# Optimization experiments

Measured on AMD Instinct MI355X. Metric: run time of the kernel, lower is better.

The kernel has to match this reference:

```python
import jax, jax.numpy as jnp
import numpy as np

L, H, Wn, C = 2048, 768, 1024, 64


def setup_inputs() -> dict:
    key = jax.random.key(0)
    ks = jax.random.split(key, 12)
    s = 1.0 / np.sqrt(H)
    s3 = 1.0 / np.sqrt(3 * H)
    return {
        "tok_embs": jax.random.normal(ks[0], (L, H), jnp.float32),
        "wmask": jax.random.randint(ks[1], (L,), 0, Wn + 1),  # 1-indexed word positions, 0 = ignore
        "text_length": Wn,
        "label_embs": jax.random.normal(ks[2], (C, H), jnp.float32),
        "W_tok": jax.random.normal(ks[3], (H, 2 * H), jnp.float32) * s,
        "b_tok": jnp.zeros((2 * H,), jnp.float32),
        "W_lab": jax.random.normal(ks[4], (H, 2 * H), jnp.float32) * s,
        "b_lab": jnp.zeros((2 * H,), jnp.float32),
        "W1": jax.random.normal(ks[5], (3 * H, H), jnp.float32) * s3,
        "b1": jnp.zeros((H,), jnp.float32),
        "W2": jax.random.normal(ks[6], (H, 3), jnp.float32) * s,
        "b2": jnp.zeros((3,), jnp.float32),
    }


def reference(tok_embs, wmask, text_length, label_embs, W_tok, b_tok, W_lab, b_lab, W1, b1, W2, b2):
    Wd = text_length
    Hd = tok_embs.shape[-1]
    # --- word-level scatter pooling: we[wmask-1] = tok_embs where wmask > 0 ---
    # route masked-out tokens to a dummy row Wd, then drop it (jit-safe, no nonzero)
    tgt = jnp.where(wmask > 0, wmask - 1, Wd)
    we = jnp.zeros((Wd + 1, Hd), tok_embs.dtype).at[tgt].set(tok_embs)[:Wd]  # (W, H)
    # --- scorer ---
    t = (we @ W_tok + b_tok).reshape(Wd, 2, Hd)        # (W, 2, H)
    lb = (label_embs @ W_lab + b_lab).reshape(-1, 2, Hd)  # (C, 2, H)
    Cd = lb.shape[0]
    t0 = jnp.broadcast_to(t[:, None, 0, :], (Wd, Cd, Hd))
    l0 = jnp.broadcast_to(lb[None, :, 0, :], (Wd, Cd, Hd))
    prod = t[:, None, 1, :] * lb[None, :, 1, :]        # (W, C, H)
    cat = jnp.concatenate([t0, l0, prod], axis=-1)     # (W, C, 3H)
    h = jax.nn.relu(cat @ W1 + b1)                     # (W, C, H)
    scores = h @ W2 + b2                               # (W, C, 3)
    return scores
```

## Files before the change

kernel.cpp:

```cpp
#include <hip/hip_runtime.h>
#include <hip/hip_bf16.h>

static constexpr int Hd = 768;
static constexpr int H2 = 1536;
static constexpr int Cn = 64;

typedef __attribute__((ext_vector_type(8))) short short8;
typedef __attribute__((ext_vector_type(8))) _Float16 half8;
typedef __attribute__((ext_vector_type(4))) float f32x4;
typedef unsigned short us;

__device__ inline unsigned int f2bf2(float a, float b) {
    __hip_bfloat162 h = __float22bfloat162_rn(float2{a, b});
    return *reinterpret_cast<unsigned int*>(&h);
}

__device__ inline void split1(float x, us& h, us& l) {
    __hip_bfloat16 hb = __float2bfloat16(x);
    float hf = __bfloat162float(hb);
    __hip_bfloat16 lb_ = __float2bfloat16(x - hf);
    h = *reinterpret_cast<us*>(&hb);
    l = *reinterpret_cast<us*>(&lb_);
}

__device__ inline us f2b(float x) {
    __hip_bfloat16 b = __float2bfloat16(x);
    return *reinterpret_cast<us*>(&b);
}

__device__ inline us f2h(float x) {
    _Float16 h = (_Float16)x;
    return *reinterpret_cast<us*>(&h);
}

__device__ inline float b2f(us u) {
    __hip_bfloat16 b = *reinterpret_cast<__hip_bfloat16*>(&u);
    return __bfloat162float(b);
}

__device__ inline short8 hmul8(short8 a, short8 b) {
    half8 x = __builtin_bit_cast(half8, a);
    half8 y = __builtin_bit_cast(half8, b);
    half8 r = x * y;
    return __builtin_bit_cast(short8, r);
}

__device__ inline void gload16(const void* g, void* l) {
    __builtin_amdgcn_global_load_lds(
        (const __attribute__((address_space(1))) unsigned int*)g,
        (__attribute__((address_space(3))) unsigned int*)l, 16, 0, 0);
}

__global__ void k_init(int* widx, int Wd) {
    int i = blockIdx.x * 256 + threadIdx.x;
    if (i < Wd) widx[i] = -1;
}

__global__ void k_scatter(const int* __restrict__ wmask, int* widx, int L, int Wd) {
    int i = blockIdx.x * 256 + threadIdx.x;
    if (i < L) {
        int m = wmask[i];
        if (m > 0 && m <= Wd) atomicMax(&widx[m - 1], i);
    }
}

__global__ void k_build_we_split(const float4* __restrict__ tok, const int* __restrict__ widx,
                                 us* __restrict__ weh, us* __restrict__ wel, int Wd) {
    int i = blockIdx.x * 256 + threadIdx.x;
    if (i >= Wd * 192) return;
    int w = i / 192, c4 = i - w * 192;
    int idx = widx[w];
    float4 v = (idx >= 0) ? tok[idx * 192 + c4] : float4{0.f, 0.f, 0.f, 0.f};
    us hh[4], ll[4];
    split1(v.x, hh[0], ll[0]);
    split1(v.y, hh[1], ll[1]);
    split1(v.z, hh[2], ll[2]);
    split1(v.w, hh[3], ll[3]);
    size_t o = (size_t)w * Hd + c4 * 4;
    *(ushort4*)&weh[o] = ushort4{hh[0], hh[1], hh[2], hh[3]};
    *(ushort4*)&wel[o] = ushort4{ll[0], ll[1], ll[2], ll[3]};
}

struct TSArgs {
    const float* src[5];
    us* th[5];
    us* tl[5];
    int ld[5];
    int N[5];
    int fmt[5];
};
__global__ __launch_bounds__(256)
void k_tsplit(TSArgs a) {
    __shared__ float tile[64][65];
    const int z = blockIdx.z;
    const int n0 = blockIdx.x * 64, k0 = blockIdx.y * 64;
    if (n0 >= a.N[z]) return;
    const float* W = a.src[z];
    const int ld = a.ld[z];
    for (int idx = threadIdx.x; idx < 4096; idx += 256) {
        int kk = idx >> 6, nn = idx & 63;
        tile[kk][nn] = W[(size_t)(k0 + kk) * ld + n0 + nn];
    }
    __syncthreads();
    us* Th = a.th[z];
    us* Tl = a.tl[z];
    const int fmt = a.fmt[z];
    for (int idx = threadIdx.x; idx < 4096; idx += 256) {
        int nn = idx >> 6, kk = idx & 63;
        size_t o = (size_t)(n0 + nn) * Hd + k0 + kk;
        if (fmt) {
            Th[o] = f2h(tile[kk][nn]);
        } else {
            us h, l;
            split1(tile[kk][nn], h, l);
            Th[o] = h;
            Tl[o] = l;
        }
    }
}

__global__ __launch_bounds__(256)
void k_split(const float* __restrict__ x, int lda, int cols,
             us* __restrict__ h, us* __restrict__ l, int n4) {
    int i = blockIdx.x * 256 + threadIdx.x;
    if (i >= n4) return;
    int c4 = cols >> 2;
    int row = i / c4, cc = (i - row * c4) * 4;
    float4 v = *(const float4*)&x[(size_t)row * lda + cc];
    us hh[4], ll[4];
    split1(v.x, hh[0], ll[0]);
    split1(v.y, hh[1], ll[1]);
    split1(v.z, hh[2], ll[2]);
    split1(v.w, hh[3], ll[3]);
    size_t o = (size_t)row * cols + cc;
    *(ushort4*)&h[o] = ushort4{hh[0], hh[1], hh[2], hh[3]};
    *(ushort4*)&l[o] = ushort4{ll[0], ll[1], ll[2], ll[3]};
}

__global__ __launch_bounds__(256)
void k_gemm2(const us* __restrict__ Ah, const us* __restrict__ Al,
             const us* __restrict__ BhT, const us* __restrict__ BlT,
             float* __restrict__ Cpart, int M, int N, int K) {
    __shared__ __align__(16) us S[2][4][64 * 32];
    const int tid = threadIdx.x, wave = tid >> 6, lane = tid & 63;
    const int quad = lane >> 4, l15 = lane & 15;
    const int wm = wave & 1, wn = wave >> 1;
    const int m0 = blockIdx.y * 64, n0 = blockIdx.x * 64;
    const int Ks = K / gridDim.z, kbeg = blockIdx.z * Ks, kend = kbeg + Ks;
    float* C = Cpart + (size_t)blockIdx.z * M * N;

    const int srow = wave * 16 + (lane >> 2), soff = (lane & 3) * 8;
    const size_t gaB = (size_t)(m0 + srow) * K + soff;
    const size_t gbB = (size_t)(n0 + srow) * K + soff;
    const int lo = wave * 16 * 32;

    f32x4 acc[2][2];
#pragma unroll
    for (int a = 0; a < 2; ++a)
#pragma unroll
        for (int b = 0; b < 2; ++b) acc[a][b] = (f32x4){0.f, 0.f, 0.f, 0.f};

    auto stage = [&](int p, int k0) {
        gload16(Ah + gaB + k0, &S[p][0][lo]);
        gload16(Al + gaB + k0, &S[p][1][lo]);
        gload16(BhT + gbB + k0, &S[p][2][lo]);
        gload16(BlT + gbB + k0, &S[p][3][lo]);
    };

    int p = 0;
    stage(0, kbeg);
    for (int k0 = kbeg; k0 < kend; k0 += 32) {
        __syncthreads();
        if (k0 + 32 < kend) stage(p ^ 1, k0 + 32);
        short8 ah[2], al[2], bh[2], bl[2];
#pragma unroll
        for (int mt = 0; mt < 2; ++mt) {
            int off = (wm * 32 + mt * 16 + l15) * 32 + quad * 8;
            ah[mt] = *(const short8*)&S[p][0][off];
            al[mt] = *(const short8*)&S[p][1][off];
        }
#pragma unroll
        for (int nt = 0; nt < 2; ++nt) {
            int off = (wn * 32 + nt * 16 + l15) * 32 + quad * 8;
            bh[nt] = *(const short8*)&S[p][2][off];
            bl[nt] = *(const short8*)&S[p][3][off];
        }
#pragma unroll
        for (int mt = 0; mt < 2; ++mt)
#pragma unroll
            for (int nt = 0; nt < 2; ++nt) {
                acc[mt][nt] = __builtin_amdgcn_mfma_f32_16x16x32_bf16(al[mt], bh[nt], acc[mt][nt], 0, 0, 0);
                acc[mt][nt] = __builtin_amdgcn_mfma_f32_16x16x32_bf16(ah[mt], bl[nt], acc[mt][nt], 0, 0, 0);
                acc[mt][nt] = __builtin_amdgcn_mfma_f32_16x16x32_bf16(ah[mt], bh[nt], acc[mt][nt], 0, 0, 0);
            }
        p ^= 1;
    }
#pragma unroll
    for (int mt = 0; mt < 2; ++mt)
#pragma unroll
        for (int nt = 0; nt < 2; ++nt) {
            int col = n0 + wn * 32 + nt * 16 + l15;
#pragma unroll
            for (int reg = 0; reg < 4; ++reg) {
                int row = m0 + wm * 32 + mt * 16 + quad * 4 + reg;
                C[(size_t)row * N + col] = acc[mt][nt][reg];
            }
        }
}

__global__ __launch_bounds__(256)
void k_gemm3(const us* __restrict__ Ah, const us* __restrict__ Al,
             const us* __restrict__ BhT, const us* __restrict__ BlT,
             const float* __restrict__ bias, float* __restrict__ outF,
             us* __restrict__ sh, us* __restrict__ sl, us* __restrict__ bh16,
             int fp16out, int scols, int N, int K) {
    __shared__ __align__(16) us S[2][4][64 * 32];
    const int tid = threadIdx.x, wave = tid >> 6, lane = tid & 63;
    const int quad = lane >> 4, l15 = lane & 15;
    const int wm = wave & 1, wn = wave >> 1;
    const int m0 = blockIdx.y * 64, n0 = blockIdx.x * 64;

    const int srow = wave * 16 + (lane >> 2), soff = (lane & 3) * 8;
    const size_t gaB = (size_t)(m0 + srow) * K + soff;
    const size_t gbB = (size_t)(n0 + srow) * K + soff;
    const int lo = wave * 16 * 32;

    f32x4 acc[2][2];
#pragma unroll
    for (int a = 0; a < 2; ++a)
#pragma unroll
        for (int b = 0; b < 2; ++b) acc[a][b] = (f32x4){0.f, 0.f, 0.f, 0.f};

    auto stage = [&](int p, int k0) {
        gload16(Ah + gaB + k0, &S[p][0][lo]);
        gload16(Al + gaB + k0, &S[p][1][lo]);
        gload16(BhT + gbB + k0, &S[p][2][lo]);
        gload16(BlT + gbB + k0, &S[p][3][lo]);
    };

    int p = 0;
    stage(0, 0);
    for (int k0 = 0; k0 < K; k0 += 32) {
        __syncthreads();
        if (k0 + 32 < K) stage(p ^ 1, k0 + 32);
        short8 ah[2], al[2], bh[2], bl[2];
#pragma unroll
        for (int mt = 0; mt < 2; ++mt) {
            int off = (wm * 32 + mt * 16 + l15) * 32 + quad * 8;
            ah[mt] = *(const short8*)&S[p][0][off];
            al[mt] = *(const short8*)&S[p][1][off];
        }
#pragma unroll
        for (int nt = 0; nt < 2; ++nt) {
            int off = (wn * 32 + nt * 16 + l15) * 32 + quad * 8;
            bh[nt] = *(const short8*)&S[p][2][off];
            bl[nt] = *(const short8*)&S[p][3][off];
        }
#pragma unroll
        for (int mt = 0; mt < 2; ++mt)
#pragma unroll
            for (int nt = 0; nt < 2; ++nt) {
                acc[mt][nt] = __builtin_amdgcn_mfma_f32_16x16x32_bf16(al[mt], bh[nt], acc[mt][nt], 0, 0, 0);
                acc[mt][nt] = __builtin_amdgcn_mfma_f32_16x16x32_bf16(ah[mt], bl[nt], acc[mt][nt], 0, 0, 0);
                acc[mt][nt] = __builtin_amdgcn_mfma_f32_16x16x32_bf16(ah[mt], bh[nt], acc[mt][nt], 0, 0, 0);
            }
        p ^= 1;
    }
#pragma unroll
    for (int mt = 0; mt < 2; ++mt)
#pragma unroll
        for (int nt = 0; nt < 2; ++nt) {
            int col = n0 + wn * 32 + nt * 16 + l15;
            float bb = bias ? bias[col] : 0.f;
#pragma unroll
            for (int reg = 0; reg < 4; ++reg) {
                int row = m0 + wm * 32 + mt * 16 + quad * 4 + reg;
                float v = acc[mt][nt][reg] + bb;
                if (outF) outF[(size_t)row * N + col] = v;
                if (sh) {
                    if (col < scols) {
                        us h, l;
                        split1(v, h, l);
                        size_t o = (size_t)row * scols + col;
                        sh[o] = h;
                        sl[o] = l;
                    } else if (bh16) {
                        bh16[(size_t)row * scols + (col - scols)] = fp16out ? f2h(v) : f2b(v);
                    }
                }
            }
        }
}

__global__ __launch_bounds__(256)
void k_reduce(const float* __restrict__ part, int S, int MN, int N,
              const float* __restrict__ bias, float* __restrict__ outF,
              us* __restrict__ sh, us* __restrict__ sl, int scols,
              us* __restrict__ bh16, int fp16out) {
    int i = blockIdx.x * 256 + threadIdx.x;
    if (i >= MN) return;
    float v = 0.f;
    for (int s = 0; s < S; ++s) v += part[(size_t)s * MN + i];
    int row = i / N, col = i - row * N;
    if (bias) v += bias[col];
    if (outF) outF[i] = v;
    if (col < scols) {
        if (sh) {
            us h, l;
            split1(v, h, l);
            size_t o = (size_t)row * scols + col;
            sh[o] = h;
            sl[o] = l;
        }
    } else if (bh16) {
        bh16[(size_t)row * scols + (col - scols)] = fp16out ? f2h(v) : f2b(v);
    }
}

__global__ __launch_bounds__(256, 2)
void k_mfma9(const us* __restrict__ t1b,
             const us* __restrict__ W1ct,
             const us* __restrict__ lb1b,
             const float* __restrict__ Aw,
             const float* __restrict__ Bc,
             const float* __restrict__ W2,
             float* __restrict__ scr) {
    __shared__ __align__(16) us As[3][4096];
    __shared__ __align__(16) us Bs[3][4096];
    __shared__ __align__(16) us lbs[2][Hd];
    __shared__ float sred[2 * 128 * 3];

    const int tid = threadIdx.x, wave = tid >> 6, lane = tid & 63;
    const int quad = lane >> 4, l15 = lane & 15;
    const int wm = wave & 1, wn = wave >> 1;

    const int b = blockIdx.x;
    const int xcd = b & 7, slot = b >> 3;
    const int jx = slot >> 5;
    const int cp = slot & 31;
    const int c0 = cp * 2;
    const int jt = jx * 128, m0 = xcd * 128;

    for (int i = tid; i < 2 * 128 * 3; i += 256) sred[i] = 0.f;
    if (tid < 192) {
        int cc = tid / 96, o = (tid - cc * 96) * 8;
        *(short8*)&lbs[cc][o] = *(const short8*)&lb1b[(size_t)(c0 + cc) * Hd + o];
    }

    const int srow = (wave & 1) * 64 + lane;
    const int skq = (wave >> 1) * 8;
    const us* gA = W1ct + (size_t)(jt + srow) * Hd + skq;
    const us* gB = t1b + (size_t)(m0 + srow) * Hd + skq;

    f32x4 acc0[4][4], acc1[4][4];
#pragma unroll
    for (int mt = 0; mt < 4; ++mt)
#pragma unroll
        for (int nt = 0; nt < 4; ++nt) {
            acc0[mt][nt] = (f32x4){0.f, 0.f, 0.f, 0.f};
            acc1[mt][nt] = (f32x4){0.f, 0.f, 0.f, 0.f};
        }

    auto stage = [&](int p, int k0) {
        gload16(gA + k0,      &As[p][wave * 512]);
        gload16(gA + k0 + 16, &As[p][(wave + 4) * 512]);
        gload16(gB + k0,      &Bs[p][wave * 512]);
        gload16(gB + k0 + 16, &Bs[p][(wave + 4) * 512]);
    };

    const int rbA = quad * 1024 + (wm * 64 + l15) * 8;
    const int rbB = quad * 1024 + (wn * 64 + l15) * 8;

    __syncthreads();

    stage(0, 0);
    stage(1, 32);
    int p = 0;
    for (int k0 = 0; k0 < Hd; k0 += 32) {
        if (k0 + 32 < Hd) asm volatile("s_waitcnt vmcnt(4)" ::: "memory");
        else              asm volatile("s_waitcnt vmcnt(0)" ::: "memory");
        __builtin_amdgcn_s_barrier();
        __builtin_amdgcn_sched_barrier(0);
        if (k0 + 64 < Hd) {
            int nb = p + 2; if (nb >= 3) nb -= 3;
            stage(nb, k0 + 64);
        }
        short8 af[4], bf[4];
#pragma unroll
        for (int mt = 0; mt < 4; ++mt) af[mt] = *(const short8*)&As[p][rbA + mt * 128];
#pragma unroll
        for (int nt = 0; nt < 4; ++nt) bf[nt] = *(const short8*)&Bs[p][rbB + nt * 128];
        short8 lv0 = *(const short8*)&lbs[0][k0 + quad * 8];
        short8 lv1 = *(const short8*)&lbs[1][k0 + quad * 8];
        __builtin_amdgcn_s_setprio(1);
#pragma unroll
        for (int mt = 0; mt < 4; ++mt) {
            short8 a0 = hmul8(af[mt], lv0);
            short8 a1 = hmul8(af[mt], lv1);
#pragma unroll
            for (int nt = 0; nt < 4; ++nt) {
                acc0[mt][nt] = __builtin_amdgcn_mfma_f32_16x16x32_f16(
                    __builtin_bit_cast(half8, a0),
                    __builtin_bit_cast(half8, bf[nt]), acc0[mt][nt], 0, 0, 0);
                acc1[mt][nt] = __builtin_amdgcn_mfma_f32_16x16x32_f16(
                    __builtin_bit_cast(half8, a1),
                    __builtin_bit_cast(half8, bf[nt]), acc1[mt][nt], 0, 0, 0);
            }
        }
        __builtin_amdgcn_s_setprio(0);
        p = (p + 1 < 3) ? p + 1 : 0;
    }

    float bcv0[4][4], bcv1[4][4], w2v[4][4][3];
#pragma unroll
    for (int mt = 0; mt < 4; ++mt) {
        const int jb = jt + wm * 64 + mt * 16 + quad * 4;
        float4 b4 = *(const float4*)&Bc[(size_t)c0 * Hd + jb];
        bcv0[mt][0] = b4.x; bcv0[mt][1] = b4.y; bcv0[mt][2] = b4.z; bcv0[mt][3] = b4.w;
        float4 b5 = *(const float4*)&Bc[(size_t)(c0 + 1) * Hd + jb];
        bcv1[mt][0] = b5.x; bcv1[mt][1] = b5.y; bcv1[mt][2] = b5.z; bcv1[mt][3] = b5.w;
#pragma unroll
        for (int reg = 0; reg < 4; ++reg)
#pragma unroll
            for (int r = 0; r < 3; ++r) w2v[mt][reg][r] = W2[(jb + reg) * 3 + r];
    }

    auto reduce_c = [&](const f32x4 (&ac)[4][4], const float (&bcv)[4][4], int cc) {
#pragma unroll
        for (int nt = 0; nt < 4; ++nt) {
            const int w = m0 + wn * 64 + nt * 16 + l15;
            const float* awp = Aw + (size_t)w * Hd + jt + wm * 64;
            float s0 = 0.f, s1 = 0.f, s2 = 0.f;
#pragma unroll
            for (int mt = 0; mt < 4; ++mt) {
                float4 a4 = *(const float4*)&awp[mt * 16 + quad * 4];
                float av[4] = {a4.x, a4.y, a4.z, a4.w};
#pragma unroll
                for (int reg = 0; reg < 4; ++reg) {
                    float h = ac[mt][nt][reg] + av[reg] + bcv[mt][reg];
                    h = h > 0.f ? h : 0.f;
                    s0 += h * w2v[mt][reg][0];
                    s1 += h * w2v[mt][reg][1];
                    s2 += h * w2v[mt][reg][2];
                }
            }
            s0 += __shfl_xor(s0, 16); s0 += __shfl_xor(s0, 32);
            s1 += __shfl_xor(s1, 16); s1 += __shfl_xor(s1, 32);
            s2 += __shfl_xor(s2, 16); s2 += __shfl_xor(s2, 32);
            if (quad == 0) {
                const int wl = wn * 64 + nt * 16 + l15;
                atomicAdd(&sred[cc * 384 + wl * 3 + 0], s0);
                atomicAdd(&sred[cc * 384 + wl * 3 + 1], s1);
                atomicAdd(&sred[cc * 384 + wl * 3 + 2], s2);
            }
        }
    };
    reduce_c(acc0, bcv0, 0);
    reduce_c(acc1, bcv1, 1);
    __syncthreads();

    float* slab = scr + ((size_t)jx * 1024 * Cn + (size_t)m0 * Cn) * 3;
    for (int i = tid; i < 2 * 128 * 3; i += 256) {
        int cc = i / 384, j = i - cc * 384;
        int wl = j / 3, r = j - wl * 3;
        slab[((size_t)wl * Cn + (c0 + cc)) * 3 + r] = sred[i];
    }
}

__global__ __launch_bounds__(256)
void k_scores(const float* __restrict__ scr, const float* __restrict__ b2,
              float* __restrict__ out, int n) {
    int i = blockIdx.x * 256 + threadIdx.x;
    if (i >= n) return;
    float v = b2[i % 3];
#pragma unroll
    for (int s = 0; s < 6; ++s) v += scr[(size_t)s * n + i];
    out[i] = v;
}

extern "C" void kernel_launch(void* const* d_in, const int* in_sizes, int n_in,
                              void* d_out, int out_size, void* d_ws, size_t ws_size,
                              hipStream_t stream) {
    const float* tok    = (const float*)d_in[0];
    const int*   wmask  = (const int*)d_in[1];
    const float* labe   = (const float*)d_in[3];
    const float* W_tok  = (const float*)d_in[4];
    const float* b_tok  = (const float*)d_in[5];
    const float* W_lab  = (const float*)d_in[6];
    const float* b_lab  = (const float*)d_in[7];
    const float* W1     = (const float*)d_in[8];
    const float* b1     = (const float*)d_in[9];
    const float* W2     = (const float*)d_in[10];
    const float* b2     = (const float*)d_in[11];
    float* out = (float*)d_out;

    const int L  = in_sizes[1];
    const int Wd = out_size / (Cn * 3);

    char* ws = (char*)d_ws;
    size_t off = 0;
    auto alloc = [&](size_t bytes) { char* p = ws + off; off += (bytes + 255) & ~(size_t)255; return p; };
    int*   widx  = (int*)alloc(4096);
    float* Abuf  = (float*)alloc((size_t)Wd * Hd * 4);
    float* Bbuf  = (float*)alloc((size_t)Cn * Hd * 4);
    us* W1ct  = (us*)alloc((size_t)Hd * Hd * 2);
    us* W1cl  = (us*)alloc((size_t)Hd * Hd * 2);
    us* t1b   = (us*)alloc((size_t)Wd * Hd * 2);
    us* lb1b  = (us*)alloc((size_t)Cn * Hd * 2);
    float* scr = (float*)alloc((size_t)6 * Wd * Cn * 3 * 4);
    us* WtTh  = (us*)alloc((size_t)H2 * Hd * 2);
    us* WtTl  = (us*)alloc((size_t)H2 * Hd * 2);
    us* WlTh  = (us*)alloc((size_t)H2 * Hd * 2);
    us* WlTl  = (us*)alloc((size_t)H2 * Hd * 2);
    us* W1aTh = (us*)alloc((size_t)Hd * Hd * 2);
    us* W1aTl = (us*)alloc((size_t)Hd * Hd * 2);
    us* W1bTh = (us*)alloc((size_t)Hd * Hd * 2);
    us* W1bTl = (us*)alloc((size_t)Hd * Hd * 2);
    us* weh   = (us*)alloc((size_t)Wd * Hd * 2);
    us* wel   = (us*)alloc((size_t)Wd * Hd * 2);
    us* lah   = (us*)alloc((size_t)Cn * Hd * 2);
    us* lal   = (us*)alloc((size_t)Cn * Hd * 2);
    us* t0h   = (us*)alloc((size_t)Wd * Hd * 2);
    us* t0l   = (us*)alloc((size_t)Wd * Hd * 2);
    us* lb0h  = (us*)alloc((size_t)Cn * Hd * 2);
    us* lb0l  = (us*)alloc((size_t)Cn * Hd * 2);
    float* part = (float*)alloc((size_t)8 * Cn * H2 * 4);

    k_init<<<(Wd + 255) / 256, 256, 0, stream>>>(widx, Wd);
    k_scatter<<<(L + 255) / 256, 256, 0, stream>>>(wmask, widx, L, Wd);
    k_build_we_split<<<(Wd * 192 + 255) / 256, 256, 0, stream>>>((const float4*)tok, widx, weh, wel, Wd);

    TSArgs ts;
    ts.src[0] = W_tok;  ts.th[0] = WtTh;  ts.tl[0] = WtTl;  ts.ld[0] = H2; ts.N[0] = H2; ts.fmt[0] = 0;
    ts.src[1] = W_lab;  ts.th[1] = WlTh;  ts.tl[1] = WlTl;  ts.ld[1] = H2; ts.N[1] = H2; ts.fmt[1] = 0;
    ts.src[2] = W1;                         ts.th[2] = W1aTh; ts.tl[2] = W1aTl; ts.ld[2] = Hd; ts.N[2] = Hd; ts.fmt[2] = 0;
    ts.src[3] = W1 + (size_t)Hd * Hd;       ts.th[3] = W1bTh; ts.tl[3] = W1bTl; ts.ld[3] = Hd; ts.N[3] = Hd; ts.fmt[3] = 0;
    ts.src[4] = W1 + (size_t)2 * Hd * Hd;   ts.th[4] = W1ct;  ts.tl[4] = W1cl;  ts.ld[4] = Hd; ts.N[4] = Hd; ts.fmt[4] = 1;
    k_tsplit<<<dim3(H2 / 64, Hd / 64, 5), 256, 0, stream>>>(ts);

    k_split<<<(Cn * Hd / 4 + 255) / 256, 256, 0, stream>>>(labe, Hd, Hd, lah, lal, Cn * Hd / 4);

    k_gemm3<<<dim3(H2 / 64, Wd / 64), 256, 0, stream>>>(weh, wel, WtTh, WtTl, b_tok,
                                                        nullptr, t0h, t0l, t1b, 1, Hd, H2, Hd);

    k_gemm2<<<dim3(H2 / 64, 1, 8), 256, 0, stream>>>(lah, lal, WlTh, WlTl, part, Cn, H2, Hd);
    k_reduce<<<(Cn * H2 + 255) / 256, 256, 0, stream>>>(part, 8, Cn * H2, H2, b_lab, nullptr, lb0h, lb0l, Hd, lb1b, 1);

    k_gemm3<<<dim3(Hd / 64, Wd / 64), 256, 0, stream>>>(t0h, t0l, W1aTh, W1aTl, nullptr,
                                                        Abuf, nullptr, nullptr, nullptr, 0, 0, Hd, Hd);

    k_gemm2<<<dim3(Hd / 64, 1, 8), 256, 0, stream>>>(lb0h, lb0l, W1bTh, W1bTl, part, Cn, Hd, Hd);
    k_reduce<<<(Cn * Hd + 255) / 256, 256, 0, stream>>>(part, 8, Cn * Hd, Hd, b1, Bbuf, nullptr, nullptr, Hd, nullptr, 0);

    k_mfma9<<<1536, 256, 0, stream>>>(t1b, W1ct, lb1b, Abuf, Bbuf, W2, scr);

    k_scores<<<(Wd * Cn * 3 + 255) / 256, 256, 0, stream>>>(scr, b2, out, Wd * Cn * 3);
}
```

Before: 259.0 us.

## Double-buffer MFMA operand fragments in registers to overlap LDS reads with compute

Restructures the fused W1c MFMA kernel's K loop into a two-stage register ping-pong. The next tile's A/B/label fragments are read from LDS, and the following global tile is staged, before the current tile's MFMA cluster runs. The goal is to hide LDS read latency behind matrix instructions. In exchange, the global wait changes from vmcnt(4) to vmcnt(0), so only one tile is prefetched ahead instead of two. The extra fragment registers also raise VGPR pressure under the two-blocks-per-CU launch bound.

```diff
diff --git a/kernel.cpp b/kernel.cpp
--- a/kernel.cpp
+++ b/kernel.cpp
@@ -318,13 +318,13 @@
 }
 
 __global__ __launch_bounds__(256, 2)
-void k_mfma9(const us* __restrict__ t1b,
-             const us* __restrict__ W1ct,
-             const us* __restrict__ lb1b,
-             const float* __restrict__ Aw,
-             const float* __restrict__ Bc,
-             const float* __restrict__ W2,
-             float* __restrict__ scr) {
+void k_mfma10(const us* __restrict__ t1b,
+              const us* __restrict__ W1ct,
+              const us* __restrict__ lb1b,
+              const float* __restrict__ Aw,
+              const float* __restrict__ Bc,
+              const float* __restrict__ W2,
+              float* __restrict__ scr) {
     __shared__ __align__(16) us As[3][4096];
     __shared__ __align__(16) us Bs[3][4096];
     __shared__ __align__(16) us lbs[2][Hd];
@@ -361,7 +361,7 @@
             acc1[mt][nt] = (f32x4){0.f, 0.f, 0.f, 0.f};
         }
 
-    auto stage = [&](int p, int k0) {
+    auto stageT = [&](int p, int k0) {
         gload16(gA + k0,      &As[p][wave * 512]);
         gload16(gA + k0 + 16, &As[p][(wave + 4) * 512]);
         gload16(gB + k0,      &Bs[p][wave * 512]);
@@ -371,32 +371,25 @@
     const int rbA = quad * 1024 + (wm * 64 + l15) * 8;
     const int rbB = quad * 1024 + (wn * 64 + l15) * 8;
 
-    __syncthreads();
-
-    stage(0, 0);
-    stage(1, 32);
-    int p = 0;
-    for (int k0 = 0; k0 < Hd; k0 += 32) {
-        if (k0 + 32 < Hd) asm volatile("s_waitcnt vmcnt(4)" ::: "memory");
-        else              asm volatile("s_waitcnt vmcnt(0)" ::: "memory");
-        __builtin_amdgcn_s_barrier();
-        __builtin_amdgcn_sched_barrier(0);
-        if (k0 + 64 < Hd) {
-            int nb = p + 2; if (nb >= 3) nb -= 3;
-            stage(nb, k0 + 64);
-        }
-        short8 af[4], bf[4];
-#pragma unroll
-        for (int mt = 0; mt < 4; ++mt) af[mt] = *(const short8*)&As[p][rbA + mt * 128];
-#pragma unroll
-        for (int nt = 0; nt < 4; ++nt) bf[nt] = *(const short8*)&Bs[p][rbB + nt * 128];
-        short8 lv0 = *(const short8*)&lbs[0][k0 + quad * 8];
-        short8 lv1 = *(const short8*)&lbs[1][k0 + quad * 8];
+    auto readFrags = [&](short8 (&af)[4], short8 (&bf)[4], short8& l0, short8& l1,
+                         int buf, int k0) {
+        const us* Ab = &As[buf][0];
+        const us* Bb = &Bs[buf][0];
+#pragma unroll
+        for (int mt = 0; mt < 4; ++mt) af[mt] = *(const short8*)&Ab[rbA + mt * 128];
+#pragma unroll
+        for (int nt = 0; nt < 4; ++nt) bf[nt] = *(const short8*)&Bb[rbB + nt * 128];
+        l0 = *(const short8*)&lbs[0][k0 + quad * 8];
+        l1 = *(const short8*)&lbs[1][k0 + quad * 8];
+    };
+
+    auto cluster = [&](const short8 (&af)[4], const short8 (&bf)[4],
+                       const short8& l0, const short8& l1) {
         __builtin_amdgcn_s_setprio(1);
 #pragma unroll
         for (int mt = 0; mt < 4; ++mt) {
-            short8 a0 = hmul8(af[mt], lv0);
-            short8 a1 = hmul8(af[mt], lv1);
+            short8 a0 = hmul8(af[mt], l0);
+            short8 a1 = hmul8(af[mt], l1);
 #pragma unroll
             for (int nt = 0; nt < 4; ++nt) {
                 acc0[mt][nt] = __builtin_amdgcn_mfma_f32_16x16x32_f16(
@@ -408,7 +401,42 @@
             }
         }
         __builtin_amdgcn_s_setprio(0);
-        p = (p + 1 < 3) ? p + 1 : 0;
+    };
+
+    __syncthreads();
+
+    stageT(0, 0);
+    stageT(1, 32);
+    asm volatile("s_waitcnt vmcnt(4)" ::: "memory");
+    __builtin_amdgcn_s_barrier();
+    __builtin_amdgcn_sched_barrier(0);
+
+    short8 afA[4], bfA[4], lvA0, lvA1;
+    short8 afB[4], bfB[4], lvB0, lvB1;
+    readFrags(afA, bfA, lvA0, lvA1, 0, 0);
+
+    int bc = 0, bn = 1, bs = 2;
+    for (int i = 0; i < 24; i += 2) {
+        if (i + 1 < 24) {
+            asm volatile("s_waitcnt vmcnt(0)" ::: "memory");
+            __builtin_amdgcn_s_barrier();
+            __builtin_amdgcn_sched_barrier(0);
+            readFrags(afB, bfB, lvB0, lvB1, bn, (i + 1) * 32);
+            if (i + 2 < 24) stageT(bs, (i + 2) * 32);
+            int t = bc; bc = bn; bn = bs; bs = t;
+            __builtin_amdgcn_sched_barrier(0);
+        }
+        cluster(afA, bfA, lvA0, lvA1);
+        if (i + 2 < 24) {
+            asm volatile("s_waitcnt vmcnt(0)" ::: "memory");
+            __builtin_amdgcn_s_barrier();
+            __builtin_amdgcn_sched_barrier(0);
+            readFrags(afA, bfA, lvA0, lvA1, bn, (i + 2) * 32);
+            if (i + 3 < 24) stageT(bs, (i + 3) * 32);
+            int t = bc; bc = bn; bn = bs; bs = t;
+            __builtin_amdgcn_sched_barrier(0);
+        }
+        cluster(afB, bfB, lvB0, lvB1);
     }
 
     float bcv0[4][4], bcv1[4][4], w2v[4][4][3];
@@ -552,7 +580,7 @@
     k_gemm2<<<dim3(Hd / 64, 1, 8), 256, 0, stream>>>(lb0h, lb0l, W1bTh, W1bTl, part, Cn, Hd, Hd);
     k_reduce<<<(Cn * Hd + 255) / 256, 256, 0, stream>>>(part, 8, Cn * Hd, Hd, b1, Bbuf, nullptr, nullptr, Hd, nullptr, 0);
 
-    k_mfma9<<<1536, 256, 0, stream>>>(t1b, W1ct, lb1b, Abuf, Bbuf, W2, scr);
+    k_mfma10<<<1536, 256, 0, stream>>>(t1b, W1ct, lb1b, Abuf, Bbuf, W2, scr);
 
     k_scores<<<(Wd * Cn * 3 + 255) / 256, 256, 0, stream>>>(scr, b2, out, Wd * Cn * 3);
 }
```

Measured after the change: 250.4 us. 1.03x faster.
